# Kernel tuning notes

Hardware: AMD Instinct MI355X
Metric: run time of the kernel (lower is better)

The kernel has to match this reference:

```python
import jax, jax.numpy as jnp
import numpy as np

B, N, D = 1, 4096, 3072
H, DH = 16, 64
INNER = H * DH  # 1024
SCALE = DH ** -0.5
EPS = 1e-5


def setup_inputs() -> dict:
    key = jax.random.key(0)
    ks = jax.random.split(key, 4)
    x = jax.random.normal(ks[0], (B, N, D), jnp.float32)
    pe = jax.random.normal(ks[1], (1, 1, N, DH // 2, 2, 2), jnp.float32)
    w_qkv = jax.random.normal(ks[2], (3 * INNER, D), jnp.float32) * 0.02
    w_out = jax.random.normal(ks[3], (D, INNER), jnp.float32) * 0.02
    ln_g = jnp.ones((D,), jnp.float32)
    ln_b = jnp.zeros((D,), jnp.float32)
    return {"x": x, "pe": pe, "w_qkv": w_qkv, "w_out": w_out, "ln_g": ln_g, "ln_b": ln_b}


def _apply_rope(t, pe):
    # t: [b,h,n,d], pe: [1,1,n,d/2,2,2] (Flux rope layout)
    b, h, n, d = t.shape
    t_ = t.reshape(b, h, n, d // 2, 1, 2)
    out = pe[..., 0] * t_[..., 0] + pe[..., 1] * t_[..., 1]  # [b,h,n,d/2,2]
    return out.reshape(b, h, n, d)


def reference(x, pe, w_qkv, w_out, ln_g, ln_b):
    # LayerNorm (norm2)
    mu = jnp.mean(x, axis=-1, keepdims=True)
    var = jnp.mean((x - mu) ** 2, axis=-1, keepdims=True)
    xn = (x - mu) / jnp.sqrt(var + EPS) * ln_g + ln_b
    # QKV projection (no bias)
    qkv = xn @ w_qkv.T  # [b,n,3*inner]
    q, k, v = jnp.split(qkv, 3, axis=-1)
    def split_heads(t):
        return t.reshape(B, N, H, DH).transpose(0, 2, 1, 3)  # b h n d
    q, k, v = split_heads(q), split_heads(k), split_heads(v)
    # RoPE on q and k (attention_aug_bbox with mask=None, aug idx = -1 -> plain rope attn)
    q = _apply_rope(q, pe)
    k = _apply_rope(k, pe)
    scores = jnp.einsum('bhqd,bhkd->bhqk', q, k) * SCALE
    attn = jax.nn.softmax(scores, axis=-1)
    o = jnp.einsum('bhqk,bhkd->bhqd', attn, v)
    o = o.transpose(0, 2, 1, 3).reshape(B, N, INNER)  # b n (h d)
    return o @ w_out.T  # [b,n,dim]
```

## Files before the change

kernel.cpp:

```cpp
#include <hip/hip_runtime.h>
#include <hip/hip_bf16.h>

typedef unsigned short u16;
typedef __attribute__((ext_vector_type(8))) short bf16x8;
typedef __attribute__((ext_vector_type(4))) float f32x4;

#define N_TOK 4096
#define DMODEL 3072
#define NH 16
#define DHEAD 64
#define INNER 1024
#define SCALE_LOG2E 0.18033688011112042f

__device__ __forceinline__ u16 f2bf(float f) {
    union { float f; unsigned u; } un; un.f = f;
    unsigned r = un.u + 0x7fffu + ((un.u >> 16) & 1u);
    return (u16)(r >> 16);
}
__device__ __forceinline__ float bf2f(u16 u) {
    union { unsigned u; float f; } x; x.u = ((unsigned)u) << 16; return x.f;
}
__device__ __forceinline__ unsigned pk2bf(float a, float b) {
    union { float f; unsigned u; } ua, ub; ua.f = a; ub.f = b;
    return __builtin_amdgcn_perm(ub.u + 0x8000u, ua.u + 0x8000u, 0x07060302u);
}
__device__ __forceinline__ void load_lds16(const u16* g, u16* l) {
    __builtin_amdgcn_global_load_lds(
        (const __attribute__((address_space(1))) unsigned int*)g,
        (__attribute__((address_space(3))) unsigned int*)l, 16, 0, 0);
}

__global__ __launch_bounds__(256) void ln_kernel(const float* __restrict__ x,
                                                 const float* __restrict__ g,
                                                 const float* __restrict__ b,
                                                 u16* __restrict__ xn) {
    int row = blockIdx.x;
    int tid = threadIdx.x;
    const float4* xr = (const float4*)(x + (size_t)row * DMODEL);
    float4 v[3];
    float s = 0.f, ss = 0.f;
#pragma unroll
    for (int i = 0; i < 3; ++i) {
        v[i] = xr[i * 256 + tid];
        s  += v[i].x + v[i].y + v[i].z + v[i].w;
        ss += v[i].x * v[i].x + v[i].y * v[i].y + v[i].z * v[i].z + v[i].w * v[i].w;
    }
#pragma unroll
    for (int off = 32; off; off >>= 1) {
        s  += __shfl_xor(s, off);
        ss += __shfl_xor(ss, off);
    }
    __shared__ float red[8];
    int wid = tid >> 6, lane = tid & 63;
    if (lane == 0) { red[wid] = s; red[wid + 4] = ss; }
    __syncthreads();
    s  = red[0] + red[1] + red[2] + red[3];
    ss = red[4] + red[5] + red[6] + red[7];
    float mean = s * (1.f / DMODEL);
    float var  = ss * (1.f / DMODEL) - mean * mean;
    float rstd = rsqrtf(var + 1e-5f);
    ushort4* orow = (ushort4*)(xn + (size_t)row * DMODEL);
#pragma unroll
    for (int i = 0; i < 3; ++i) {
        float4 gg = ((const float4*)g)[i * 256 + tid];
        float4 bb = ((const float4*)b)[i * 256 + tid];
        ushort4 o;
        o.x = f2bf((v[i].x - mean) * rstd * gg.x + bb.x);
        o.y = f2bf((v[i].y - mean) * rstd * gg.y + bb.y);
        o.z = f2bf((v[i].z - mean) * rstd * gg.z + bb.z);
        o.w = f2bf((v[i].w - mean) * rstd * gg.w + bb.w);
        orow[i * 256 + tid] = o;
    }
}

__global__ __launch_bounds__(256) void cvt_bf16(const float* __restrict__ in,
                                                u16* __restrict__ out, int n4) {
    int i = blockIdx.x * 256 + threadIdx.x;
    if (i < n4) {
        float4 v = ((const float4*)in)[i];
        ushort4 o;
        o.x = f2bf(v.x); o.y = f2bf(v.y); o.z = f2bf(v.z); o.w = f2bf(v.w);
        ((ushort4*)out)[i] = o;
    }
}

template <int CBF16>
__global__ __launch_bounds__(256) void gemm_bt(const u16* __restrict__ A,
                                               const u16* __restrict__ B,
                                               void* __restrict__ C,
                                               int M, int Nn, int K) {
    __shared__ u16 As[128 * 32];
    __shared__ u16 Bs[128 * 32];
    int tid = threadIdx.x;
    int lane = tid & 63, wid = tid >> 6;
    int wm = wid >> 1, wn = wid & 1;
    int l15 = lane & 15, quad = lane >> 4;
    int m0 = blockIdx.y * 128, n0 = blockIdx.x * 128;

    f32x4 zero4 = {0.f, 0.f, 0.f, 0.f};
    f32x4 acc[4][4];
#pragma unroll
    for (int i = 0; i < 4; ++i)
#pragma unroll
        for (int j = 0; j < 4; ++j) acc[i][j] = zero4;

    const u16* Ab = A + (size_t)m0 * K;
    const u16* Bb = B + (size_t)n0 * K;
    int row0 = tid >> 2, c0 = (((tid & 3) ^ ((lane >> 3) & 3)) * 8);
    int row1 = row0 + 64;
    int rsw = (l15 >> 1) & 3;

    for (int k0 = 0; k0 < K; k0 += 32) {
        load_lds16(Ab + (size_t)row0 * K + k0 + c0, &As[wid * 512]);
        load_lds16(Ab + (size_t)row1 * K + k0 + c0, &As[2048 + wid * 512]);
        load_lds16(Bb + (size_t)row0 * K + k0 + c0, &Bs[wid * 512]);
        load_lds16(Bb + (size_t)row1 * K + k0 + c0, &Bs[2048 + wid * 512]);
        __syncthreads();
        bf16x8 a[4], b[4];
#pragma unroll
        for (int t = 0; t < 4; ++t) {
            a[t] = *(const bf16x8*)&As[(wm * 64 + t * 16 + l15) * 32 + ((quad ^ rsw) * 8)];
            b[t] = *(const bf16x8*)&Bs[(wn * 64 + t * 16 + l15) * 32 + ((quad ^ rsw) * 8)];
        }
#pragma unroll
        for (int mt = 0; mt < 4; ++mt)
#pragma unroll
            for (int nt = 0; nt < 4; ++nt)
                acc[mt][nt] = __builtin_amdgcn_mfma_f32_16x16x32_bf16(a[mt], b[nt], acc[mt][nt], 0, 0, 0);
        __syncthreads();
    }
#pragma unroll
    for (int mt = 0; mt < 4; ++mt)
#pragma unroll
        for (int nt = 0; nt < 4; ++nt)
#pragma unroll
            for (int r = 0; r < 4; ++r) {
                int rr = m0 + wm * 64 + mt * 16 + quad * 4 + r;
                int cc = n0 + wn * 64 + nt * 16 + l15;
                if (CBF16)
                    ((u16*)C)[(size_t)rr * Nn + cc] = f2bf(acc[mt][nt][r]);
                else
                    ((float*)C)[(size_t)rr * Nn + cc] = acc[mt][nt][r];
            }
}

__global__ __launch_bounds__(256) void rope_qk(const u16* __restrict__ qkv,
                                               const float* __restrict__ pe,
                                               u16* __restrict__ Qr,
                                               u16* __restrict__ Kr) {
    int n = blockIdx.x;
    int tid = threadIdx.x;
    const u16* qrow = qkv + (size_t)n * DMODEL;
    const float4* pen = (const float4*)(pe + (size_t)n * 128);
#pragma unroll
    for (int it = 0; it < 2; ++it) {
        int p = it * 256 + tid;
        int h = p >> 5, i = p & 31;
        float4 w = pen[i];
        size_t obase = ((size_t)h * N_TOK + n) * DHEAD + 2 * i;
        unsigned qq = *(const unsigned*)&qrow[h * 64 + 2 * i];
        float q0 = bf2f((u16)qq), q1 = bf2f((u16)(qq >> 16));
        *(unsigned*)&Qr[obase] = pk2bf((w.x * q0 + w.y * q1) * SCALE_LOG2E,
                                       (w.z * q0 + w.w * q1) * SCALE_LOG2E);
        unsigned kk = *(const unsigned*)&qrow[INNER + h * 64 + 2 * i];
        float k0 = bf2f((u16)kk), k1 = bf2f((u16)(kk >> 16));
        *(unsigned*)&Kr[obase] = pk2bf(w.x * k0 + w.y * k1, w.z * k0 + w.w * k1);
    }
}

__global__ __launch_bounds__(256) void v_transpose(const u16* __restrict__ qkv,
                                                   u16* __restrict__ Vt) {
    __shared__ u16 t[64][65];
    int n0 = blockIdx.x * 64;
    int h = blockIdx.y;
    int tid = threadIdx.x;
#pragma unroll
    for (int it = 0; it < 4; ++it) {
        int nr = it * 16 + (tid >> 4);
        int dc = (tid & 15) * 4;
        ushort4 v = *(const ushort4*)&qkv[(size_t)(n0 + nr) * DMODEL + 2 * INNER + h * 64 + dc];
        t[dc + 0][nr] = v.x; t[dc + 1][nr] = v.y; t[dc + 2][nr] = v.z; t[dc + 3][nr] = v.w;
    }
    __syncthreads();
#pragma unroll
    for (int it = 0; it < 4; ++it) {
        int dr = it * 16 + (tid >> 4);
        int nc = (tid & 15) * 4;
        ushort4 v;
        v.x = t[dr][nc]; v.y = t[dr][nc + 1]; v.z = t[dr][nc + 2]; v.w = t[dr][nc + 3];
        *(ushort4*)&Vt[((size_t)h * 64 + dr) * N_TOK + n0 + nc] = v;
    }
}

__global__ __launch_bounds__(256, 2) void flash_attn(const u16* __restrict__ Q,
                                                     const u16* __restrict__ K,
                                                     const u16* __restrict__ Vt,
                                                     u16* __restrict__ O) {
    __shared__ u16 lds_all[16384];
    u16* Ks = lds_all;
    u16* Vs = lds_all + 4096;
    int tid = threadIdx.x, lane = tid & 63, wid = tid >> 6;
    u16* Ps = lds_all + 8192 + wid * 2048;
    int l15 = lane & 15, quad = lane >> 4;
    int sw = l15 & 7;
    int h = blockIdx.y;
    int q0 = blockIdx.x * 128 + wid * 32;
    const u16* Qh = Q + (size_t)h * N_TOK * DHEAD;
    const u16* Kh = K + (size_t)h * N_TOK * DHEAD;
    const u16* Vh = Vt + (size_t)h * DHEAD * N_TOK;

    f32x4 zero4 = {0.f, 0.f, 0.f, 0.f};
    bf16x8 ones;
#pragma unroll
    for (int i = 0; i < 8; ++i) ones[i] = (short)0x3F80;

    bf16x8 aq[2][2];
#pragma unroll
    for (int mtQ = 0; mtQ < 2; ++mtQ)
#pragma unroll
        for (int kc = 0; kc < 2; ++kc)
            aq[mtQ][kc] = *(const bf16x8*)&Qh[(size_t)(q0 + mtQ * 16 + l15) * DHEAD + kc * 32 + quad * 8];

    f32x4 o[2][4], lacc[2];
#pragma unroll
    for (int mtQ = 0; mtQ < 2; ++mtQ) {
#pragma unroll
        for (int dt = 0; dt < 4; ++dt) o[mtQ][dt] = zero4;
        lacc[mtQ] = zero4;
    }

    int rbase = wid * 16;
    int rowoff = lane >> 3;
    int csw = ((lane & 7) ^ rowoff) * 8;

    for (int kt = 0; kt < N_TOK; kt += 64) {
        load_lds16(&Kh[(size_t)(kt + rbase + rowoff) * DHEAD + csw], &Ks[rbase * 64]);
        load_lds16(&Kh[(size_t)(kt + rbase + 8 + rowoff) * DHEAD + csw], &Ks[(rbase + 8) * 64]);
        load_lds16(&Vh[(size_t)(rbase + rowoff) * N_TOK + kt + csw], &Vs[rbase * 64]);
        load_lds16(&Vh[(size_t)(rbase + 8 + rowoff) * N_TOK + kt + csw], &Vs[(rbase + 8) * 64]);
        __syncthreads();

        bf16x8 bk[4][2], av[4][2];
#pragma unroll
        for (int t = 0; t < 4; ++t)
#pragma unroll
            for (int kc = 0; kc < 2; ++kc) {
                int off = (t * 16 + l15) * 64 + (((kc * 4 + quad) ^ sw) * 8);
                bk[t][kc] = *(const bf16x8*)&Ks[off];
                av[t][kc] = *(const bf16x8*)&Vs[off];
            }
        __syncthreads();

#pragma unroll
        for (int mtQ = 0; mtQ < 2; ++mtQ) {
            f32x4 s[4];
#pragma unroll
            for (int ntK = 0; ntK < 4; ++ntK) {
                f32x4 t0 = __builtin_amdgcn_mfma_f32_16x16x32_bf16(bk[ntK][0], aq[mtQ][0], zero4, 0, 0, 0);
                s[ntK] = __builtin_amdgcn_mfma_f32_16x16x32_bf16(bk[ntK][1], aq[mtQ][1], t0, 0, 0, 0);
            }
#pragma unroll
            for (int ntK = 0; ntK < 4; ++ntK) {
                uint2 pv;
                pv.x = pk2bf(__builtin_amdgcn_exp2f(s[ntK][0]), __builtin_amdgcn_exp2f(s[ntK][1]));
                pv.y = pk2bf(__builtin_amdgcn_exp2f(s[ntK][2]), __builtin_amdgcn_exp2f(s[ntK][3]));
                int pc = (ntK * 2 + (quad >> 1)) ^ sw;
                *(uint2*)&Ps[(mtQ * 16 + l15) * 64 + pc * 8 + (quad & 1) * 4] = pv;
            }
            bf16x8 bp0 = *(const bf16x8*)&Ps[(mtQ * 16 + l15) * 64 + ((quad ^ sw) * 8)];
            bf16x8 bp1 = *(const bf16x8*)&Ps[(mtQ * 16 + l15) * 64 + (((4 + quad) ^ sw) * 8)];
            lacc[mtQ] = __builtin_amdgcn_mfma_f32_16x16x32_bf16(ones, bp0, lacc[mtQ], 0, 0, 0);
            lacc[mtQ] = __builtin_amdgcn_mfma_f32_16x16x32_bf16(ones, bp1, lacc[mtQ], 0, 0, 0);
#pragma unroll
            for (int dt = 0; dt < 4; ++dt) {
                o[mtQ][dt] = __builtin_amdgcn_mfma_f32_16x16x32_bf16(av[dt][0], bp0, o[mtQ][dt], 0, 0, 0);
                o[mtQ][dt] = __builtin_amdgcn_mfma_f32_16x16x32_bf16(av[dt][1], bp1, o[mtQ][dt], 0, 0, 0);
            }
        }
    }

    __syncthreads();
    u16* scratch = lds_all + wid * 2048;
#pragma unroll
    for (int mtQ = 0; mtQ < 2; ++mtQ) {
        float rl = 1.f / lacc[mtQ][0];
#pragma unroll
        for (int dt = 0; dt < 4; ++dt) {
            uint2 ov;
            ov.x = pk2bf(o[mtQ][dt][0] * rl, o[mtQ][dt][1] * rl);
            ov.y = pk2bf(o[mtQ][dt][2] * rl, o[mtQ][dt][3] * rl);
            *(uint2*)&scratch[(mtQ * 16 + l15) * 64 + dt * 16 + quad * 4] = ov;
        }
    }
#pragma unroll
    for (int p = 0; p < 4; ++p) {
        int q_local = p * 8 + (lane >> 3);
        int dcol = (lane & 7) * 8;
        bf16x8 v = *(const bf16x8*)&scratch[q_local * 64 + dcol];
        *(bf16x8*)&O[(size_t)(q0 + q_local) * INNER + h * 64 + dcol] = v;
    }
}

extern "C" void kernel_launch(void* const* d_in, const int* in_sizes, int n_in,
                              void* d_out, int out_size, void* d_ws, size_t ws_size,
                              hipStream_t stream) {
    const float* x     = (const float*)d_in[0];
    const float* pe    = (const float*)d_in[1];
    const float* w_qkv = (const float*)d_in[2];
    const float* w_out = (const float*)d_in[3];
    const float* ln_g  = (const float*)d_in[4];
    const float* ln_b  = (const float*)d_in[5];
    float* out = (float*)d_out;

    char* ws = (char*)d_ws;
    u16* xn  = (u16*)ws;  ws += (size_t)N_TOK * DMODEL * 2;
    u16* wq  = (u16*)ws;  ws += (size_t)3 * INNER * DMODEL * 2;
    u16* wo  = (u16*)ws;  ws += (size_t)DMODEL * INNER * 2;
    u16* qkv = (u16*)ws;  ws += (size_t)N_TOK * DMODEL * 2;
    u16* Qr  = (u16*)ws;  ws += (size_t)NH * N_TOK * DHEAD * 2;
    u16* Kr  = (u16*)ws;  ws += (size_t)NH * N_TOK * DHEAD * 2;
    u16* Vt  = (u16*)ws;  ws += (size_t)NH * DHEAD * N_TOK * 2;
    u16* Ob  = (u16*)ws;  ws += (size_t)N_TOK * INNER * 2;

    ln_kernel<<<N_TOK, 256, 0, stream>>>(x, ln_g, ln_b, xn);
    {
        int n4 = 3 * INNER * DMODEL / 4;
        cvt_bf16<<<(n4 + 255) / 256, 256, 0, stream>>>(w_qkv, wq, n4);
    }
    {
        int n4 = DMODEL * INNER / 4;
        cvt_bf16<<<(n4 + 255) / 256, 256, 0, stream>>>(w_out, wo, n4);
    }
    gemm_bt<1><<<dim3(DMODEL / 128, N_TOK / 128), 256, 0, stream>>>(xn, wq, qkv, N_TOK, DMODEL, DMODEL);
    rope_qk<<<N_TOK, 256, 0, stream>>>(qkv, pe, Qr, Kr);
    v_transpose<<<dim3(N_TOK / 64, NH), 256, 0, stream>>>(qkv, Vt);
    flash_attn<<<dim3(N_TOK / 128, NH), 256, 0, stream>>>(Qr, Kr, Vt, Ob);
    gemm_bt<0><<<dim3(DMODEL / 128, N_TOK / 128), 256, 0, stream>>>(Ob, wo, out, N_TOK, DMODEL, INNER);
}
```

Baseline: 402.5 us.

## Replace 128x128 GEMM with pipelined 256x256 double-buffered 8-wave GEMM

Replaces the simple 128x128 single-buffered bf16 GEMM with a 256x256-tile, 512-thread kernel. It double-buffers K=64 slices in 128KB of LDS and interleaves direct-to-LDS global loads with MFMA phases, using explicit waitcnt, barriers and setprio. It also adds an XCD-aware block-index remap for L2 locality. The aim is to hide memory latency and raise arithmetic intensity for both projection GEMMs, at the cost of heavy LDS use, lower occupancy and fragile hand-tuned synchronization.

```diff
diff --git a/kernel.cpp b/kernel.cpp
--- a/kernel.cpp
+++ b/kernel.cpp
@@ -84,63 +84,134 @@
     }
 }
 
+
+#define VM6 asm volatile("s_waitcnt vmcnt(6)" ::: "memory")
+#define VM0 asm volatile("s_waitcnt vmcnt(0)" ::: "memory")
+#define LGK8 asm volatile("s_waitcnt lgkmcnt(8)" ::: "memory")
+#define NOPS ((void)0)
+
+#define ST_A(d, h, t) do { \
+    load_lds16(pA##h##0 + (size_t)(t) * 64, &lds[(d) * 16384 + (h) * 8192 + dq]); \
+    load_lds16(pA##h##1 + (size_t)(t) * 64, &lds[(d) * 16384 + (h) * 8192 + dq + 512]); \
+  } while (0)
+#define ST_B(d, h, t) do { \
+    load_lds16(pB##h##0 + (size_t)(t) * 64, &lds[32768 + (d) * 16384 + (h) * 8192 + dq]); \
+    load_lds16(pB##h##1 + (size_t)(t) * 64, &lds[32768 + (d) * 16384 + (h) * 8192 + dq + 512]); \
+  } while (0)
+
+#define PHASE(d, p, STAGE, PRE, POST) do { \
+    bf16x8 afr[2][2]; \
+    if ((p) == 0) { \
+      _Pragma("unroll") for (int nf = 0; nf < 4; ++nf) { \
+        bfr[nf][0] = *(const bf16x8*)&lds[(d) * 16384 + baseB + nf * 1024 + c0]; \
+        bfr[nf][1] = *(const bf16x8*)&lds[(d) * 16384 + baseB + nf * 1024 + c1]; \
+      } \
+    } \
+    _Pragma("unroll") for (int mfl = 0; mfl < 2; ++mfl) { \
+      afr[mfl][0] = *(const bf16x8*)&lds[(d) * 16384 + (p) * 4096 + mfl * 1024 + baseA + c0]; \
+      afr[mfl][1] = *(const bf16x8*)&lds[(d) * 16384 + (p) * 4096 + mfl * 1024 + baseA + c1]; \
+    } \
+    STAGE; \
+    PRE; \
+    __builtin_amdgcn_s_barrier(); \
+    asm volatile("s_waitcnt lgkmcnt(0)" ::: "memory"); \
+    __builtin_amdgcn_sched_barrier(0); \
+    __builtin_amdgcn_s_setprio(1); \
+    _Pragma("unroll") for (int mfl = 0; mfl < 2; ++mfl) \
+      _Pragma("unroll") for (int nf = 0; nf < 4; ++nf) { \
+        acc[(p) * 2 + mfl][nf] = __builtin_amdgcn_mfma_f32_16x16x32_bf16(afr[mfl][0], bfr[nf][0], acc[(p) * 2 + mfl][nf], 0, 0, 0); \
+        acc[(p) * 2 + mfl][nf] = __builtin_amdgcn_mfma_f32_16x16x32_bf16(afr[mfl][1], bfr[nf][1], acc[(p) * 2 + mfl][nf], 0, 0, 0); \
+      } \
+    __builtin_amdgcn_s_setprio(0); \
+    POST; \
+    __builtin_amdgcn_s_barrier(); \
+  } while (0)
+
 template <int CBF16>
-__global__ __launch_bounds__(256) void gemm_bt(const u16* __restrict__ A,
-                                               const u16* __restrict__ B,
-                                               void* __restrict__ C,
-                                               int M, int Nn, int K) {
-    __shared__ u16 As[128 * 32];
-    __shared__ u16 Bs[128 * 32];
-    int tid = threadIdx.x;
-    int lane = tid & 63, wid = tid >> 6;
-    int wm = wid >> 1, wn = wid & 1;
-    int l15 = lane & 15, quad = lane >> 4;
-    int m0 = blockIdx.y * 128, n0 = blockIdx.x * 128;
-
+__global__ __launch_bounds__(512, 2) void gemm256(const u16* __restrict__ A,
+                                                  const u16* __restrict__ B,
+                                                  void* __restrict__ C,
+                                                  int M, int Nn, int K) {
+    __shared__ u16 lds[65536];
+    const int tid = threadIdx.x;
+    const int lane = tid & 63, wid = tid >> 6;
+    const int wm = wid >> 2, wn = wid & 3;
+    const int l15 = lane & 15, quad = lane >> 4;
+    const int sw = l15 & 7;
+
+    int nbx = Nn >> 8;
+    int cpx = gridDim.x >> 3;
+    int wg = (blockIdx.x & 7) * cpx + (blockIdx.x >> 3);
+    int m0 = (wg / nbx) << 8, n0 = (wg % nbx) << 8;
+
+    const int baseA = wm * 2048 + l15 * 64;
+    const int baseB = 32768 + wn * 4096 + l15 * 64;
+    const int c0 = (quad ^ sw) * 8;
+    const int c1 = ((4 + quad) ^ sw) * 8;
+    const int dq = wid * 1024;
+
+    const u16 *pA00, *pA01, *pA10, *pA11, *pB00, *pB01, *pB10, *pB11;
+    {
+        int scol = ((lane & 7) ^ (lane >> 3)) * 8;
+#define MKSRC(h, j, PA, PB) { \
+        int ell = (h) * 128 + (wid * 2 + (j)) * 8 + (lane >> 3); \
+        int g = ell >> 6, wmh = (ell >> 5) & 1, r = ell & 31; \
+        PA = A + (size_t)(m0 + wmh * 128 + g * 32 + r) * K + scol; \
+        PB = B + (size_t)(n0 + ell) * K + scol; }
+        MKSRC(0, 0, pA00, pB00) MKSRC(0, 1, pA01, pB01)
+        MKSRC(1, 0, pA10, pB10) MKSRC(1, 1, pA11, pB11)
+#undef MKSRC
+    }
+
+    f32x4 acc[8][4];
     f32x4 zero4 = {0.f, 0.f, 0.f, 0.f};
-    f32x4 acc[4][4];
-#pragma unroll
-    for (int i = 0; i < 4; ++i)
+#pragma unroll
+    for (int i = 0; i < 8; ++i)
 #pragma unroll
         for (int j = 0; j < 4; ++j) acc[i][j] = zero4;
-
-    const u16* Ab = A + (size_t)m0 * K;
-    const u16* Bb = B + (size_t)n0 * K;
-    int row0 = tid >> 2, c0 = (((tid & 3) ^ ((lane >> 3) & 3)) * 8);
-    int row1 = row0 + 64;
-    int rsw = (l15 >> 1) & 3;
-
-    for (int k0 = 0; k0 < K; k0 += 32) {
-        load_lds16(Ab + (size_t)row0 * K + k0 + c0, &As[wid * 512]);
-        load_lds16(Ab + (size_t)row1 * K + k0 + c0, &As[2048 + wid * 512]);
-        load_lds16(Bb + (size_t)row0 * K + k0 + c0, &Bs[wid * 512]);
-        load_lds16(Bb + (size_t)row1 * K + k0 + c0, &Bs[2048 + wid * 512]);
-        __syncthreads();
-        bf16x8 a[4], b[4];
-#pragma unroll
-        for (int t = 0; t < 4; ++t) {
-            a[t] = *(const bf16x8*)&As[(wm * 64 + t * 16 + l15) * 32 + ((quad ^ rsw) * 8)];
-            b[t] = *(const bf16x8*)&Bs[(wn * 64 + t * 16 + l15) * 32 + ((quad ^ rsw) * 8)];
-        }
-#pragma unroll
-        for (int mt = 0; mt < 4; ++mt)
-#pragma unroll
-            for (int nt = 0; nt < 4; ++nt)
-                acc[mt][nt] = __builtin_amdgcn_mfma_f32_16x16x32_bf16(a[mt], b[nt], acc[mt][nt], 0, 0, 0);
-        __syncthreads();
-    }
-#pragma unroll
-    for (int mt = 0; mt < 4; ++mt)
-#pragma unroll
-        for (int nt = 0; nt < 4; ++nt)
+    bf16x8 bfr[4][2];
+
+    ST_B(0, 0, 0); ST_B(0, 1, 0); ST_A(0, 0, 0); ST_A(0, 1, 0);
+    ST_B(1, 0, 1); ST_B(1, 1, 1); ST_A(1, 0, 1);
+    VM6;
+    __builtin_amdgcn_s_barrier();
+
+    const int NIT = (K >> 7) - 1;
+    for (int i = 0; i < NIT; ++i) {
+        int t = 2 * i;
+        PHASE(0, 0, ST_A(1, 1, t + 1), LGK8, NOPS);
+        PHASE(0, 1, ST_B(0, 0, t + 2), NOPS, NOPS);
+        PHASE(0, 2, ST_B(0, 1, t + 2), NOPS, NOPS);
+        PHASE(0, 3, ST_A(0, 0, t + 2), NOPS, VM6);
+        PHASE(1, 0, ST_A(0, 1, t + 2), LGK8, NOPS);
+        PHASE(1, 1, ST_B(1, 0, t + 3), NOPS, NOPS);
+        PHASE(1, 2, ST_B(1, 1, t + 3), NOPS, NOPS);
+        PHASE(1, 3, ST_A(1, 0, t + 3), NOPS, VM6);
+    }
+    {
+        int T = K >> 6;
+        PHASE(0, 0, ST_A(1, 1, T - 1), LGK8, NOPS);
+        PHASE(0, 1, NOPS, NOPS, NOPS);
+        PHASE(0, 2, NOPS, NOPS, NOPS);
+        PHASE(0, 3, NOPS, NOPS, VM0);
+        PHASE(1, 0, NOPS, LGK8, NOPS);
+        PHASE(1, 1, NOPS, NOPS, NOPS);
+        PHASE(1, 2, NOPS, NOPS, NOPS);
+        PHASE(1, 3, NOPS, NOPS, NOPS);
+    }
+
+#pragma unroll
+    for (int mf = 0; mf < 8; ++mf)
+#pragma unroll
+        for (int nf = 0; nf < 4; ++nf)
 #pragma unroll
             for (int r = 0; r < 4; ++r) {
-                int rr = m0 + wm * 64 + mt * 16 + quad * 4 + r;
-                int cc = n0 + wn * 64 + nt * 16 + l15;
+                int rr = m0 + wm * 128 + mf * 16 + quad * 4 + r;
+                int cc = n0 + wn * 64 + nf * 16 + l15;
                 if (CBF16)
-                    ((u16*)C)[(size_t)rr * Nn + cc] = f2bf(acc[mt][nt][r]);
+                    ((u16*)C)[(size_t)rr * Nn + cc] = f2bf(acc[mf][nf][r]);
                 else
-                    ((float*)C)[(size_t)rr * Nn + cc] = acc[mt][nt][r];
+                    ((float*)C)[(size_t)rr * Nn + cc] = acc[mf][nf][r];
             }
 }
 
@@ -331,9 +402,9 @@
         int n4 = DMODEL * INNER / 4;
         cvt_bf16<<<(n4 + 255) / 256, 256, 0, stream>>>(w_out, wo, n4);
     }
-    gemm_bt<1><<<dim3(DMODEL / 128, N_TOK / 128), 256, 0, stream>>>(xn, wq, qkv, N_TOK, DMODEL, DMODEL);
+    gemm256<1><<<dim3((N_TOK / 256) * (DMODEL / 256)), 512, 0, stream>>>(xn, wq, qkv, N_TOK, DMODEL, DMODEL);
     rope_qk<<<N_TOK, 256, 0, stream>>>(qkv, pe, Qr, Kr);
     v_transpose<<<dim3(N_TOK / 64, NH), 256, 0, stream>>>(qkv, Vt);
     flash_attn<<<dim3(N_TOK / 128, NH), 256, 0, stream>>>(Qr, Kr, Vt, Ob);
-    gemm_bt<0><<<dim3(DMODEL / 128, N_TOK / 128), 256, 0, stream>>>(Ob, wo, out, N_TOK, DMODEL, INNER);
-}
+    gemm256<0><<<dim3((N_TOK / 256) * (DMODEL / 256)), 512, 0, stream>>>(Ob, wo, out, N_TOK, DMODEL, INNER);
+}
```

Result: faster. 375.4 us (-6.7%).
